# Kernel tuning notes

Hardware: AMD Instinct MI355X
Metric: run time of the kernel (lower is better)

## Reference

```python
import jax, jax.numpy as jnp
import numpy as np

T, B, H = 512, 64, 512
GRAD_CLIP = 1.0


def setup_inputs() -> dict:
    key = jax.random.key(0)
    k_x, k_r, k_wi, k_wh = jax.random.split(key, 4)
    xs = jax.random.normal(k_x, (T, B, H), dtype=jnp.float32)
    resets = jax.random.randint(k_r, (T, B), 0, 2).astype(bool)
    c0 = jnp.zeros((B, H), dtype=jnp.float32)
    h0 = jnp.zeros((B, H), dtype=jnp.float32)
    scale = 1.0 / np.sqrt(H)
    # fused gate weights, gate order [i, f, g, o] (flax LSTMCell convention)
    Wi = jax.random.normal(k_wi, (H, 4 * H), dtype=jnp.float32) * scale
    Wh = jax.random.normal(k_wh, (H, 4 * H), dtype=jnp.float32) * scale
    # flax LSTMCell: input dense has no bias, hidden dense has bias with
    # forget-gate bias initialized to ones
    b = jnp.zeros((4 * H,), dtype=jnp.float32).at[H:2 * H].set(1.0)
    return {"xs": xs, "resets": resets, "c0": c0, "h0": h0,
            "Wi": Wi, "Wh": Wh, "b": b}


def _clip_st(t):
    # straight-through clip: forward value is clipped, gradient is identity
    return t + jax.lax.stop_gradient(jnp.clip(t, -GRAD_CLIP, GRAD_CLIP) - t)


def reference(xs, resets, c0, h0, Wi, Wh, b):
    def step(carry, inp):
        c, h = carry
        x, r = inp  # x: [B,H], r: [B] bool
        m = r[:, None]
        c = jnp.where(m, jnp.zeros_like(c), c)
        h = jnp.where(m, jnp.zeros_like(h), h)
        z = x @ Wi + h @ Wh + b  # [B, 4H]
        i, f, g, o = jnp.split(z, 4, axis=-1)
        i = jax.nn.sigmoid(i)
        f = jax.nn.sigmoid(f)
        g = jnp.tanh(g)
        o = jax.nn.sigmoid(o)
        nc = f * c + i * g
        nh = o * jnp.tanh(nc)
        nc = _clip_st(nc)
        nh = _clip_st(nh)  # y == clipped new_h; clipping is idempotent on values
        return (nc, nh), nh

    (cf, hf), ys = jax.lax.scan(step, (c0, h0), (xs, resets))
    return ys  # [T, B, H]
```

## Files before the change

### kernel.cpp

```cpp
#include <hip/hip_runtime.h>

#define T_ 512
#define B_ 64
#define H_ 512
#define LMAX 20
#define NROWS (T_*B_)

typedef _Float16 f16;
typedef __attribute__((ext_vector_type(2))) _Float16 f16x2;
typedef __attribute__((ext_vector_type(8))) _Float16 f16x8;
typedef __attribute__((ext_vector_type(4))) float fx4;

#define M_CNT 0
#define M_OFF 32

__device__ __forceinline__ float sigm(float z)  { return 1.0f / (1.0f + __expf(-z)); }
__device__ __forceinline__ float tanha(float z) { return 2.0f / (1.0f + __expf(-2.0f * z)) - 1.0f; }

__global__ __launch_bounds__(256) void k_prepw(const float* __restrict__ Wi,
                                               const float* __restrict__ Wh,
                                               f16* __restrict__ W2t) {
    __shared__ float tile[64][65];
    const int c0  = blockIdx.x * 64;
    const int k20 = blockIdx.y * 64;
    const int tid = threadIdx.x;
    #pragma unroll
    for (int s = 0; s < 16; s++) {
        int k2r = s * 4 + (tid >> 6);
        int c   = tid & 63;
        int k2  = k20 + k2r;
        float v = (k2 < H_) ? Wi[(size_t)k2 * 2048 + c0 + c]
                            : Wh[(size_t)(k2 - H_) * 2048 + c0 + c];
        tile[c][k2r] = v;
    }
    __syncthreads();
    const int c  = tid >> 2;
    const int ch = tid & 3;
    f16 tmp[16];
    #pragma unroll
    for (int u = 0; u < 16; u++) tmp[u] = (f16)tile[c][ch * 16 + u];
    f16* dst = W2t + (size_t)(c0 + c) * 1024 + k20 + ch * 16;
    *(uint4*)(dst)     = *(const uint4*)(tmp);
    *(uint4*)(dst + 8) = *(const uint4*)(tmp + 8);
}

__global__ __launch_bounds__(256) void k_scan_build(const int* __restrict__ resets,
                                                    int* __restrict__ lvl,
                                                    int* __restrict__ meta,
                                                    int* __restrict__ rowid,
                                                    int* __restrict__ rmap) {
    __shared__ unsigned long long mask[T_];
    __shared__ int cnt[LMAX + 1][B_];
    __shared__ int cur[LMAX + 1][B_];
    __shared__ int cntk[LMAX + 1], offk[LMAX + 1];

    const int tid  = threadIdx.x;
    const int lane = tid & 63;
    const int wave = tid >> 6;

    for (int t = wave; t < T_; t += 4) {
        int r = resets[t * B_ + lane];
        unsigned long long m = __ballot(r != 0);
        if (lane == 0) mask[t] = m;
    }
    for (int i = tid; i < (LMAX + 1) * B_; i += 256) ((int*)cnt)[i] = 0;
    __syncthreads();

    if (tid < B_) {
        const int b = tid;
        int prev = 0;
        for (int t = 0; t < T_; t++) {
            int rst = (int)((mask[t] >> b) & 1ULL);
            int lv = (t == 0) ? 0 : (rst ? 0 : prev + 1);
            int kk = lv < LMAX ? lv : LMAX;
            cnt[kk][b] += 1;
            lvl[t * B_ + b] = lv;
            prev = lv;
        }
    }
    __syncthreads();

    if (tid <= LMAX) {
        const int k = tid;
        int acc = 0;
        for (int b = 0; b < B_; b++) { cur[k][b] = acc; acc += cnt[k][b]; }
        cntk[k] = acc;
    }
    __syncthreads();
    if (tid == 0) {
        int acc = 0;
        for (int k = 0; k <= LMAX; k++) { offk[k] = acc; acc += cntk[k]; }
    }
    __syncthreads();
    if (tid <= LMAX) {
        const int k = tid;
        for (int b = 0; b < B_; b++) cur[k][b] += offk[k];
        meta[M_CNT + k] = cntk[k];
        meta[M_OFF + k] = offk[k];
    }
    __syncthreads();

    if (tid < B_) {
        const int b = tid;
        int prev = 0;
        for (int t = 0; t < T_; t++) {
            int rst = (int)((mask[t] >> b) & 1ULL);
            int lv = (t == 0) ? 0 : (rst ? 0 : prev + 1);
            int kk = lv < LMAX ? lv : LMAX;
            int r = cur[kk][b];
            cur[kk][b] = r + 1;
            int tb = t * B_ + b;
            rowid[tb] = r;
            rmap[r] = tb;
            prev = lv;
        }
    }
}


__global__ __launch_bounds__(256) void k_xcast(const float* __restrict__ xs,
                                               f16* __restrict__ X) {
    int gid = blockIdx.x * 256 + threadIdx.x;
    const float4* src = (const float4*)(xs) + (size_t)gid * 2;
    float4 a = src[0], c = src[1];
    f16x8 o;
    o[0]=(f16)a.x; o[1]=(f16)a.y; o[2]=(f16)a.z; o[3]=(f16)a.w;
    o[4]=(f16)c.x; o[5]=(f16)c.y; o[6]=(f16)c.z; o[7]=(f16)c.w;
    *(f16x8*)(X + (size_t)gid * 8) = o;
}

__global__ __launch_bounds__(256) void k_hz0(const float* __restrict__ h0,
                                             const f16* __restrict__ W2t,
                                             float* __restrict__ hz0) {
    const int b = blockIdx.x >> 3;
    const int j = ((blockIdx.x & 7) * 256) + threadIdx.x;
    __shared__ float h[H_];
    for (int k = threadIdx.x; k < H_; k += 256) h[k] = h0[b * H_ + k];
    __syncthreads();
    const f16* wr = W2t + (size_t)j * 1024 + 512;
    float acc = 0.f;
    for (int k = 0; k < H_; k += 8) {
        f16x8 w = *(const f16x8*)(wr + k);
        #pragma unroll
        for (int u = 0; u < 8; u++) acc += h[k + u] * (float)w[u];
    }
    hz0[(size_t)b * 2048 + j] = acc;
}

__global__ __launch_bounds__(256) void k_xz(const f16* __restrict__ X,
                                            const f16* __restrict__ W2t,
                                            f16* __restrict__ XZ) {
    const int r0 = blockIdx.x * 128;
    const int j0 = blockIdx.y * 128;
    __shared__ __align__(16) f16 As[128][40];
    __shared__ __align__(16) f16 Bs[128][40];
    const int tid  = threadIdx.x;
    const int lane = tid & 63;
    const int wave = tid >> 6;
    const int wm = wave & 1, wn = wave >> 1;
    const int n = lane & 15, q = lane >> 4;

    fx4 acc[4][4];
    #pragma unroll
    for (int i = 0; i < 4; i++)
        #pragma unroll
        for (int jj = 0; jj < 4; jj++) acc[i][jj] = (fx4){0.f,0.f,0.f,0.f};

    const int arow = tid >> 2, ach = tid & 3;
    const f16* xa = X + (size_t)(r0 + arow) * 512 + ach * 8;
    const f16* xb = X + (size_t)(r0 + 64 + arow) * 512 + ach * 8;
    const f16* wa = W2t + (size_t)(j0 + arow) * 1024 + ach * 8;
    const f16* wb = W2t + (size_t)(j0 + 64 + arow) * 1024 + ach * 8;

    for (int k0 = 0; k0 < 512; k0 += 32) {
        *(uint4*)(&As[arow][ach * 8])      = *(const uint4*)(xa + k0);
        *(uint4*)(&As[64 + arow][ach * 8]) = *(const uint4*)(xb + k0);
        *(uint4*)(&Bs[arow][ach * 8])      = *(const uint4*)(wa + k0);
        *(uint4*)(&Bs[64 + arow][ach * 8]) = *(const uint4*)(wb + k0);
        __syncthreads();
        f16x8 af[4], bf[4];
        #pragma unroll
        for (int mt = 0; mt < 4; mt++) af[mt] = *(const f16x8*)(&As[wm*64 + mt*16 + n][q*8]);
        #pragma unroll
        for (int nt = 0; nt < 4; nt++) bf[nt] = *(const f16x8*)(&Bs[wn*64 + nt*16 + n][q*8]);
        #pragma unroll
        for (int mt = 0; mt < 4; mt++)
            #pragma unroll
            for (int nt = 0; nt < 4; nt++)
                acc[mt][nt] = __builtin_amdgcn_mfma_f32_16x16x32_f16(af[mt], bf[nt], acc[mt][nt], 0, 0, 0);
        __syncthreads();
    }
    #pragma unroll
    for (int mt = 0; mt < 4; mt++)
        #pragma unroll
        for (int nt = 0; nt < 4; nt++)
            #pragma unroll
            for (int reg = 0; reg < 4; reg++) {
                int row = r0 + wm * 64 + mt * 16 + q * 4 + reg;
                int col = j0 + wn * 64 + nt * 16 + n;
                XZ[(size_t)row * 2048 + col] = (f16)acc[mt][nt][reg];
            }
}

__global__ __launch_bounds__(256) void k_lvl0epi(
    const f16* __restrict__ XZ, const float* __restrict__ hz0,
    const float* __restrict__ c0, const float* __restrict__ bias,
    const int* __restrict__ resets, const int* __restrict__ meta,
    const int* __restrict__ rmap, const int* __restrict__ rowid,
    f16* __restrict__ Hb, f16* __restrict__ Cb, float* __restrict__ ys)
{
    const int r = blockIdx.x;
    if (r >= meta[M_CNT + 0]) return;
    const int tb = rmap[r];
    const int t = tb >> 6, b = tb & 63;
    const bool useinit = (t == 0) && (resets[b] == 0);
    int s = -1;
    if (t + 1 < T_ && resets[tb + B_] == 0) s = rowid[tb + B_];

    const int jh = threadIdx.x * 2;
    const f16* zr = XZ + (size_t)tb * 2048;
    f16x2 vi = *(const f16x2*)(zr + jh);
    f16x2 vf = *(const f16x2*)(zr + H_ + jh);
    f16x2 vg = *(const f16x2*)(zr + 2 * H_ + jh);
    f16x2 vo = *(const f16x2*)(zr + 3 * H_ + jh);

    float nhv[2], ncv[2];
    #pragma unroll
    for (int u = 0; u < 2; u++) {
        int j = jh + u;
        float zi = (float)vi[u] + bias[j];
        float zf = (float)vf[u] + bias[H_ + j];
        float zg = (float)vg[u] + bias[2 * H_ + j];
        float zo = (float)vo[u] + bias[3 * H_ + j];
        float cp = 0.f;
        if (useinit) {
            const float* hzr = hz0 + (size_t)b * 2048;
            zi += hzr[j]; zf += hzr[H_ + j]; zg += hzr[2 * H_ + j]; zo += hzr[3 * H_ + j];
            cp = c0[b * H_ + j];
        }
        float iv = sigm(zi), fv = sigm(zf), gv = tanha(zg), ov = sigm(zo);
        float nc = fv * cp + iv * gv;
        float nh = ov * tanha(nc);
        ncv[u] = fminf(1.f, fmaxf(-1.f, nc));
        nhv[u] = fminf(1.f, fmaxf(-1.f, nh));
        ys[(size_t)tb * H_ + j] = nhv[u];
    }
    if (s >= 0) {
        f16x2 hv, cv;
        hv[0] = (f16)nhv[0]; hv[1] = (f16)nhv[1];
        cv[0] = (f16)ncv[0]; cv[1] = (f16)ncv[1];
        *(f16x2*)(Hb + (size_t)s * H_ + jh) = hv;
        *(f16x2*)(Cb + (size_t)s * H_ + jh) = cv;
    }
}

__global__ __launch_bounds__(256) void k_levelh(
    int level,
    const int* __restrict__ resets,
    const f16* __restrict__ W2t,
    const float* __restrict__ bias,
    const f16* __restrict__ XZ,
    f16* __restrict__ Hb,
    f16* __restrict__ Cb,
    const int* __restrict__ meta,
    const int* __restrict__ rmap,
    const int* __restrict__ rowid,
    float* __restrict__ ys)
{
    const int cnt = meta[M_CNT + level];
    const int row0 = blockIdx.x * 64;
    if (row0 >= cnt) return;
    const int off = meta[M_OFF + level];
    const int j0 = blockIdx.y * 64;

    __shared__ __align__(16) f16 As[64][40];
    __shared__ __align__(16) f16 Ws[256][40];

    const int tid  = threadIdx.x;
    const int lane = tid & 63;
    const int wave = tid >> 6;
    const int n = lane & 15;
    const int q = lane >> 4;

    fx4 acc[16];
    #pragma unroll
    for (int i = 0; i < 16; i++) acc[i] = (fx4){0.f, 0.f, 0.f, 0.f};

    const int ar  = tid >> 2;
    const int ach = tid & 3;
    const int gr_stage = row0 + ar;
    const int srow = off + (gr_stage < cnt ? gr_stage : 0);
    const f16* agp = Hb + (size_t)srow * H_ + ach * 8;
    const int wc = tid >> 2;

    for (int k0 = 0; k0 < 512; k0 += 32) {
        *(uint4*)(&As[ar][ach * 8]) = *(const uint4*)(agp + k0);
        #pragma unroll
        for (int s = 0; s < 4; s++) {
            const f16* wp = W2t + (size_t)(s * H_ + j0 + wc) * 1024 + 512 + k0 + ach * 8;
            *(uint4*)(&Ws[s * 64 + wc][ach * 8]) = *(const uint4*)wp;
        }
        __syncthreads();
        f16x8 a = *(const f16x8*)(&As[wave * 16 + n][q * 8]);
        #pragma unroll
        for (int ct = 0; ct < 16; ct++) {
            f16x8 bb = *(const f16x8*)(&Ws[ct * 16 + n][q * 8]);
            acc[ct] = __builtin_amdgcn_mfma_f32_16x16x32_f16(a, bb, acc[ct], 0, 0, 0);
        }
        __syncthreads();
    }

    int tbs[4], succs[4], grows[4], valids[4];
    #pragma unroll
    for (int reg = 0; reg < 4; reg++) {
        int gr = row0 + wave * 16 + q * 4 + reg;
        valids[reg] = (gr < cnt);
        int grow = off + (gr < cnt ? gr : 0);
        grows[reg] = grow;
        int tb = rmap[grow];
        tbs[reg] = tb;
        int s = -1;
        if (gr < cnt && (tb >> 6) + 1 < T_ && resets[tb + B_] == 0) s = rowid[tb + B_];
        succs[reg] = s;
    }
    #pragma unroll
    for (int jt = 0; jt < 4; jt++) {
        int j = j0 + jt * 16 + n;
        float b_i = bias[j], b_f = bias[H_ + j], b_g = bias[2 * H_ + j], b_o = bias[3 * H_ + j];
        #pragma unroll
        for (int reg = 0; reg < 4; reg++) {
            if (!valids[reg]) continue;
            const f16* zr = XZ + (size_t)tbs[reg] * 2048;
            float zi = acc[jt][reg]      + b_i + (float)zr[j];
            float zf = acc[4 + jt][reg]  + b_f + (float)zr[H_ + j];
            float zg = acc[8 + jt][reg]  + b_g + (float)zr[2 * H_ + j];
            float zo = acc[12 + jt][reg] + b_o + (float)zr[3 * H_ + j];
            float cp = (float)Cb[(size_t)grows[reg] * H_ + j];
            float iv = sigm(zi), fv = sigm(zf), gv = tanha(zg), ov = sigm(zo);
            float nc = fv * cp + iv * gv;
            float nh = ov * tanha(nc);
            float ncc = fminf(1.f, fmaxf(-1.f, nc));
            float nhc = fminf(1.f, fmaxf(-1.f, nh));
            ys[(size_t)tbs[reg] * H_ + j] = nhc;
            int s = succs[reg];
            if (s >= 0) {
                Hb[(size_t)s * H_ + j] = (f16)nhc;
                Cb[(size_t)s * H_ + j] = (f16)ncc;
            }
        }
    }
}


__global__ __launch_bounds__(256) void k_fill(const float* __restrict__ xs,
                                              const float* __restrict__ c0,
                                              const float* __restrict__ h0,
                                              const int* __restrict__ resets,
                                              const int* __restrict__ rmap,
                                              const int* __restrict__ meta,
                                              f16* __restrict__ A,
                                              f16* __restrict__ Cb) {
    int gid = blockIdx.x * 256 + threadIdx.x;
    int r = gid >> 6, seg = gid & 63;
    int tb = rmap[r];
    const float4* src = (const float4*)(xs + (size_t)tb * H_ + seg * 8);
    float4 a = src[0];
    float4 c = src[1];
    f16x8 o;
    o[0]=(f16)a.x; o[1]=(f16)a.y; o[2]=(f16)a.z; o[3]=(f16)a.w;
    o[4]=(f16)c.x; o[5]=(f16)c.y; o[6]=(f16)c.z; o[7]=(f16)c.w;
    *(f16x8*)(A + (size_t)r * 1024 + seg * 8) = o;

    if (r < meta[M_CNT + 0]) {
        int t = tb >> 6, b = tb & 63;
        bool useinit = (t == 0) && (resets[b] == 0);
        f16x8 hv, cv;
        #pragma unroll
        for (int u = 0; u < 8; u++) {
            int j = seg * 8 + u;
            hv[u] = (f16)(useinit ? h0[b * H_ + j] : 0.0f);
            cv[u] = (f16)(useinit ? c0[b * H_ + j] : 0.0f);
        }
        *(f16x8*)(A + (size_t)r * 1024 + H_ + seg * 8) = hv;
        *(f16x8*)(Cb + (size_t)r * H_ + seg * 8) = cv;
    }
}

__global__ __launch_bounds__(256) void k_level(
    int level,
    const int* __restrict__ resets,
    const f16* __restrict__ W2t,
    const float* __restrict__ bias,
    f16* __restrict__ Ab,
    f16* __restrict__ Cb,
    const int* __restrict__ meta,
    const int* __restrict__ rmap,
    const int* __restrict__ rowid,
    float* __restrict__ ys)
{
    const int cnt = meta[M_CNT + level];
    const int row0 = blockIdx.x * 64;
    if (row0 >= cnt) return;
    const int off = meta[M_OFF + level];
    const int j0 = blockIdx.y * 64;

    __shared__ __align__(16) f16 As[64][40];
    __shared__ __align__(16) f16 Ws[256][40];

    const int tid  = threadIdx.x;
    const int lane = tid & 63;
    const int wave = tid >> 6;
    const int n = lane & 15;
    const int q = lane >> 4;

    fx4 acc[16];
    #pragma unroll
    for (int i = 0; i < 16; i++) acc[i] = (fx4){0.f, 0.f, 0.f, 0.f};

    const int ar  = tid >> 2;
    const int ach = tid & 3;
    const int gr_stage = row0 + ar;
    const int srow = off + (gr_stage < cnt ? gr_stage : 0);
    const f16* agp = Ab + (size_t)srow * 1024 + ach * 8;
    const int wc = tid >> 2;

    for (int k0 = 0; k0 < 1024; k0 += 32) {
        *(uint4*)(&As[ar][ach * 8]) = *(const uint4*)(agp + k0);
        #pragma unroll
        for (int s = 0; s < 4; s++) {
            const f16* wp = W2t + (size_t)(s * H_ + j0 + wc) * 1024 + k0 + ach * 8;
            *(uint4*)(&Ws[s * 64 + wc][ach * 8]) = *(const uint4*)wp;
        }
        __syncthreads();
        f16x8 a = *(const f16x8*)(&As[wave * 16 + n][q * 8]);
        #pragma unroll
        for (int ct = 0; ct < 16; ct++) {
            f16x8 bb = *(const f16x8*)(&Ws[ct * 16 + n][q * 8]);
            acc[ct] = __builtin_amdgcn_mfma_f32_16x16x32_f16(a, bb, acc[ct], 0, 0, 0);
        }
        __syncthreads();
    }

    int tbs[4], succs[4], grows[4], valids[4];
    #pragma unroll
    for (int reg = 0; reg < 4; reg++) {
        int gr = row0 + wave * 16 + q * 4 + reg;
        valids[reg] = (gr < cnt);
        int grow = off + (gr < cnt ? gr : 0);
        grows[reg] = grow;
        int tb = rmap[grow];
        tbs[reg] = tb;
        int s = -1;
        if (gr < cnt && (tb >> 6) + 1 < T_ && resets[tb + B_] == 0) s = rowid[tb + B_];
        succs[reg] = s;
    }
    #pragma unroll
    for (int jt = 0; jt < 4; jt++) {
        int j = j0 + jt * 16 + n;
        float b_i = bias[j], b_f = bias[H_ + j], b_g = bias[2 * H_ + j], b_o = bias[3 * H_ + j];
        #pragma unroll
        for (int reg = 0; reg < 4; reg++) {
            if (!valids[reg]) continue;
            float zi = acc[jt][reg] + b_i;
            float zf = acc[4 + jt][reg] + b_f;
            float zg = acc[8 + jt][reg] + b_g;
            float zo = acc[12 + jt][reg] + b_o;
            float cp = (float)Cb[(size_t)grows[reg] * H_ + j];
            float iv = sigm(zi), fv = sigm(zf), gv = tanha(zg), ov = sigm(zo);
            float nc = fv * cp + iv * gv;
            float nh = ov * tanha(nc);
            float ncc = fminf(1.f, fmaxf(-1.f, nc));
            float nhc = fminf(1.f, fmaxf(-1.f, nh));
            ys[(size_t)tbs[reg] * H_ + j] = nhc;
            int s = succs[reg];
            if (s >= 0) {
                Ab[(size_t)s * 1024 + H_ + j] = (f16)nhc;
                Cb[(size_t)s * H_ + j] = (f16)ncc;
            }
        }
    }
}

__global__ __launch_bounds__(256) void k_cleanup(
    const float* __restrict__ xs, const float* __restrict__ Wi,
    const float* __restrict__ Wh, const float* __restrict__ bias,
    const int* __restrict__ rowid, const int* __restrict__ meta,
    const int* __restrict__ rmap,
    const f16* __restrict__ Cb, float* __restrict__ ys)
{
    const int cntL = meta[M_CNT + LMAX];
    if (cntL == 0) return;
    const int offL = meta[M_OFF + LMAX];
    const int b = blockIdx.x;
    const int tid = threadIdx.x;
    __shared__ float hs[H_], cs[H_];
    int last_t = -2;
    for (int idx = 0; idx < cntL; idx++) {
        const int tb = rmap[offL + idx];
        if ((tb & 63) != b) continue;
        const int t = tb >> 6;
        if (t != last_t + 1) {
            for (int j = tid; j < H_; j += 256) {
                hs[j] = ys[(size_t)(tb - B_) * H_ + j];
                cs[j] = (float)Cb[(size_t)rowid[tb] * H_ + j];
            }
        }
        __syncthreads();
        float nh_[2], nc_[2];
        #pragma unroll
        for (int u = 0; u < 2; u++) {
            int j = tid + u * 256;
            float zi = bias[j], zf = bias[H_ + j], zg = bias[2 * H_ + j], zo = bias[3 * H_ + j];
            const float* xr = xs + (size_t)tb * H_;
            for (int k = 0; k < H_; k++) {
                float xk = xr[k], hk = hs[k];
                zi += xk * Wi[(size_t)k * 2048 + j]          + hk * Wh[(size_t)k * 2048 + j];
                zf += xk * Wi[(size_t)k * 2048 + H_ + j]     + hk * Wh[(size_t)k * 2048 + H_ + j];
                zg += xk * Wi[(size_t)k * 2048 + 2 * H_ + j] + hk * Wh[(size_t)k * 2048 + 2 * H_ + j];
                zo += xk * Wi[(size_t)k * 2048 + 3 * H_ + j] + hk * Wh[(size_t)k * 2048 + 3 * H_ + j];
            }
            float cp = cs[j];
            float iv = sigm(zi), fv = sigm(zf), gv = tanha(zg), ov = sigm(zo);
            float nc = fv * cp + iv * gv;
            float nh = ov * tanha(nc);
            nc_[u] = fminf(1.f, fmaxf(-1.f, nc));
            nh_[u] = fminf(1.f, fmaxf(-1.f, nh));
            ys[(size_t)tb * H_ + j] = nh_[u];
        }
        __syncthreads();
        #pragma unroll
        for (int u = 0; u < 2; u++) { int j = tid + u * 256; hs[j] = nh_[u]; cs[j] = nc_[u]; }
        last_t = t;
    }
}

__global__ __launch_bounds__(256) void k_fb_init(const float* __restrict__ c0,
                                                 const float* __restrict__ h0,
                                                 float* __restrict__ cbuf,
                                                 float* __restrict__ hA) {
    int idx = blockIdx.x * 256 + threadIdx.x;
    if (idx >= B_ * H_) return;
    cbuf[idx] = c0[idx];
    hA[idx] = h0[idx];
}

__global__ __launch_bounds__(256) void k_fb_step(
    int t,
    const float* __restrict__ xs, const int* __restrict__ resets,
    const float* __restrict__ Wi, const float* __restrict__ Wh,
    const float* __restrict__ bias,
    const float* __restrict__ hin, float* __restrict__ hout,
    float* __restrict__ cbuf, float* __restrict__ ys)
{
    int idx = blockIdx.x * 256 + threadIdx.x;
    int b = idx >> 9, j = idx & 511;
    int tb = t * B_ + b;
    bool rst = resets[tb] != 0;
    float zi = bias[j], zf = bias[H_ + j], zg = bias[2 * H_ + j], zo = bias[3 * H_ + j];
    const float* xr = xs + (size_t)tb * H_;
    for (int k = 0; k < H_; k++) {
        float xk = xr[k];
        zi += xk * Wi[(size_t)k * 2048 + j];
        zf += xk * Wi[(size_t)k * 2048 + H_ + j];
        zg += xk * Wi[(size_t)k * 2048 + 2 * H_ + j];
        zo += xk * Wi[(size_t)k * 2048 + 3 * H_ + j];
    }
    if (!rst) {
        const float* hr = hin + b * H_;
        for (int k = 0; k < H_; k++) {
            float hk = hr[k];
            zi += hk * Wh[(size_t)k * 2048 + j];
            zf += hk * Wh[(size_t)k * 2048 + H_ + j];
            zg += hk * Wh[(size_t)k * 2048 + 2 * H_ + j];
            zo += hk * Wh[(size_t)k * 2048 + 3 * H_ + j];
        }
    }
    float cp = rst ? 0.f : cbuf[idx];
    float iv = sigm(zi), fv = sigm(zf), gv = tanha(zg), ov = sigm(zo);
    float nc = fv * cp + iv * gv;
    float nh = ov * tanha(nc);
    float ncc = fminf(1.f, fmaxf(-1.f, nc));
    float nhc = fminf(1.f, fmaxf(-1.f, nh));
    cbuf[idx] = ncc;
    hout[idx] = nhc;
    ys[(size_t)tb * H_ + j] = nhc;
}

extern "C" void kernel_launch(void* const* d_in, const int* in_sizes, int n_in,
                              void* d_out, int out_size, void* d_ws, size_t ws_size,
                              hipStream_t stream) {
    const float* xs    = (const float*)d_in[0];
    const int*   resets= (const int*)d_in[1];
    const float* c0    = (const float*)d_in[2];
    const float* h0    = (const float*)d_in[3];
    const float* Wi    = (const float*)d_in[4];
    const float* Wh    = (const float*)d_in[5];
    const float* bias  = (const float*)d_in[6];
    float* ys = (float*)d_out;
    char* ws = (char*)d_ws;

    const size_t A_W2T  = 0;
    const size_t A_X    = A_W2T + (size_t)4*1024*1024;
    const size_t A_XZ   = A_X   + (size_t)32*1024*1024;
    const size_t A_HB   = A_XZ  + (size_t)128*1024*1024;
    const size_t A_CB   = A_HB  + (size_t)32*1024*1024;
    const size_t A_HZ0  = A_CB  + (size_t)32*1024*1024;
    const size_t A_LVL  = A_HZ0 + (size_t)512*1024;
    const size_t A_RID  = A_LVL + 131072;
    const size_t A_RMAP = A_RID + 131072;
    const size_t A_META = A_RMAP + 131072;
    const size_t NEEDED_A = A_META + 512;

    const size_t B_A    = 0;
    const size_t B_C    = 67108864;
    const size_t B_W2T  = 100663296;
    const size_t B_LVL  = 104857600;
    const size_t B_RID  = 104988672;
    const size_t B_RMAP = 105119744;
    const size_t B_META = 105250816;
    const size_t NEEDED_B = 105251328;

    if (ws_size >= NEEDED_A) {
        f16* W2t  = (f16*)(ws + A_W2T);
        f16* X    = (f16*)(ws + A_X);
        f16* XZ   = (f16*)(ws + A_XZ);
        f16* Hb   = (f16*)(ws + A_HB);
        f16* Cb   = (f16*)(ws + A_CB);
        float* hz0= (float*)(ws + A_HZ0);
        int* lvl  = (int*)(ws + A_LVL);
        int* rid  = (int*)(ws + A_RID);
        int* rmap = (int*)(ws + A_RMAP);
        int* meta = (int*)(ws + A_META);

        k_prepw<<<dim3(32, 16), dim3(256), 0, stream>>>(Wi, Wh, W2t);
        k_scan_build<<<dim3(1), dim3(256), 0, stream>>>(resets, lvl, meta, rid, rmap);
        k_xcast<<<dim3(NROWS * 64 / 256 / 8 * 8), dim3(256), 0, stream>>>(xs, X);
        k_hz0<<<dim3(512), dim3(256), 0, stream>>>(h0, W2t, hz0);
        k_xz<<<dim3(NROWS / 128, 16), dim3(256), 0, stream>>>(X, W2t, XZ);
        k_lvl0epi<<<dim3(NROWS), dim3(256), 0, stream>>>(XZ, hz0, c0, bias, resets,
                                                         meta, rmap, rid, Hb, Cb, ys);
        for (int k = 1; k < LMAX; k++) {
            int maxr = 64 * ((512 + k) / (k + 1));
            dim3 grid((maxr + 63) / 64, 8);
            k_levelh<<<grid, dim3(256), 0, stream>>>(k, resets, W2t, bias, XZ, Hb, Cb,
                                                     meta, rmap, rid, ys);
        }
        k_cleanup<<<dim3(64), dim3(256), 0, stream>>>(xs, Wi, Wh, bias, rid, meta, rmap, Cb, ys);
    } else if (ws_size >= NEEDED_B) {
        f16* A    = (f16*)(ws + B_A);
        f16* Cb   = (f16*)(ws + B_C);
        f16* W2t  = (f16*)(ws + B_W2T);
        int* lvl  = (int*)(ws + B_LVL);
        int* rid  = (int*)(ws + B_RID);
        int* rmap = (int*)(ws + B_RMAP);
        int* meta = (int*)(ws + B_META);

        k_prepw<<<dim3(32, 16), dim3(256), 0, stream>>>(Wi, Wh, W2t);
        k_scan_build<<<dim3(1), dim3(256), 0, stream>>>(resets, lvl, meta, rid, rmap);
        k_fill<<<dim3(NROWS * 64 / 256), dim3(256), 0, stream>>>(xs, c0, h0, resets, rmap, meta, A, Cb);
        for (int k = 0; k < LMAX; k++) {
            int maxr = 64 * ((512 + k) / (k + 1));
            dim3 grid((maxr + 63) / 64, 8);
            k_level<<<grid, dim3(256), 0, stream>>>(k, resets, W2t, bias, A, Cb,
                                                    meta, rmap, rid, ys);
        }
        k_cleanup<<<dim3(64), dim3(256), 0, stream>>>(xs, Wi, Wh, bias, rid, meta, rmap, Cb, ys);
    } else {
        float* cbuf = (float*)(ws);
        float* hA   = (float*)(ws + 131072);
        float* hB   = (float*)(ws + 262144);
        k_fb_init<<<dim3(128), dim3(256), 0, stream>>>(c0, h0, cbuf, hA);
        for (int t = 0; t < T_; t++) {
            const float* hin = (t & 1) ? hB : hA;
            float* hout      = (t & 1) ? hA : hB;
            k_fb_step<<<dim3(128), dim3(256), 0, stream>>>(t, xs, resets, Wi, Wh, bias,
                                                           hin, hout, cbuf, ys);
        }
    }
}
```

Before: 850.4 us.

## Fuse level-0 epilogue and per-level recurrence kernels into one cooperative persistent kernel

Replaces the level-0 epilogue launch and the series of per-level recurrence launches with a single cooperative kernel. It processes each reset-depth level in grid-stride tiles and separates levels with grid-wide syncs. It also records the deepest non-empty level, so levels that do not occur are skipped rather than launched empty. The aim is to remove roughly twenty kernel launches and their idle gaps. In exchange it adds grid barrier costs, a smaller persistent grid per level, and host occupancy and device-property queries on every call.

```diff
diff --git a/kernel.cpp b/kernel.cpp
--- a/kernel.cpp
+++ b/kernel.cpp
@@ -1,4 +1,7 @@
 #include <hip/hip_runtime.h>
+#include <hip/hip_cooperative_groups.h>
+
+namespace cg = cooperative_groups;
 
 #define T_ 512
 #define B_ 64
@@ -13,6 +16,7 @@
 
 #define M_CNT 0
 #define M_OFF 32
+#define M_MAXL 64
 
 __device__ __forceinline__ float sigm(float z)  { return 1.0f / (1.0f + __expf(-z)); }
 __device__ __forceinline__ float tanha(float z) { return 2.0f / (1.0f + __expf(-2.0f * z)) - 1.0f; }
@@ -88,8 +92,12 @@
     }
     __syncthreads();
     if (tid == 0) {
-        int acc = 0;
-        for (int k = 0; k <= LMAX; k++) { offk[k] = acc; acc += cntk[k]; }
+        int acc = 0, ml = 0;
+        for (int k = 0; k <= LMAX; k++) {
+            offk[k] = acc; acc += cntk[k];
+            if (cntk[k] > 0) ml = k;
+        }
+        meta[M_MAXL] = ml;
     }
     __syncthreads();
     if (tid <= LMAX) {
@@ -200,6 +208,163 @@
                 int col = j0 + wn * 64 + nt * 16 + n;
                 XZ[(size_t)row * 2048 + col] = (f16)acc[mt][nt][reg];
             }
+}
+
+__global__ __launch_bounds__(256) void k_levels(
+    const int* __restrict__ resets,
+    const f16* __restrict__ W2t,
+    const float* __restrict__ bias,
+    const f16* __restrict__ XZ,
+    const float* __restrict__ hz0,
+    const float* __restrict__ c0,
+    f16* __restrict__ Hb,
+    f16* __restrict__ Cb,
+    const int* __restrict__ meta,
+    const int* __restrict__ rmap,
+    const int* __restrict__ rowid,
+    float* __restrict__ ys)
+{
+    cg::grid_group gg = cg::this_grid();
+    __shared__ __align__(16) f16 As[64][40];
+    __shared__ __align__(16) f16 Ws[256][40];
+
+    const int tid  = threadIdx.x;
+    const int lane = tid & 63;
+    const int wave = tid >> 6;
+    const int n = lane & 15;
+    const int q = lane >> 4;
+
+    {
+        const int cnt0 = meta[M_CNT + 0];
+        for (int r = blockIdx.x; r < cnt0; r += gridDim.x) {
+            const int tb = rmap[r];
+            const int t = tb >> 6, b = tb & 63;
+            const bool useinit = (t == 0) && (resets[b] == 0);
+            int s = -1;
+            if (t + 1 < T_ && resets[tb + B_] == 0) s = rowid[tb + B_];
+            const int jh = tid * 2;
+            const f16* zr = XZ + (size_t)tb * 2048;
+            f16x2 vi = *(const f16x2*)(zr + jh);
+            f16x2 vf = *(const f16x2*)(zr + H_ + jh);
+            f16x2 vg = *(const f16x2*)(zr + 2 * H_ + jh);
+            f16x2 vo = *(const f16x2*)(zr + 3 * H_ + jh);
+            float nhv[2], ncv[2];
+            #pragma unroll
+            for (int u = 0; u < 2; u++) {
+                int j = jh + u;
+                float zi = (float)vi[u] + bias[j];
+                float zf = (float)vf[u] + bias[H_ + j];
+                float zg = (float)vg[u] + bias[2 * H_ + j];
+                float zo = (float)vo[u] + bias[3 * H_ + j];
+                float cp = 0.f;
+                if (useinit) {
+                    const float* hzr = hz0 + (size_t)b * 2048;
+                    zi += hzr[j]; zf += hzr[H_ + j]; zg += hzr[2 * H_ + j]; zo += hzr[3 * H_ + j];
+                    cp = c0[b * H_ + j];
+                }
+                float iv = sigm(zi), fv = sigm(zf), gv = tanha(zg), ov = sigm(zo);
+                float nc = fv * cp + iv * gv;
+                float nh = ov * tanha(nc);
+                ncv[u] = fminf(1.f, fmaxf(-1.f, nc));
+                nhv[u] = fminf(1.f, fmaxf(-1.f, nh));
+                ys[(size_t)tb * H_ + j] = nhv[u];
+            }
+            if (s >= 0) {
+                f16x2 hv, cv;
+                hv[0] = (f16)nhv[0]; hv[1] = (f16)nhv[1];
+                cv[0] = (f16)ncv[0]; cv[1] = (f16)ncv[1];
+                *(f16x2*)(Hb + (size_t)s * H_ + jh) = hv;
+                *(f16x2*)(Cb + (size_t)s * H_ + jh) = cv;
+            }
+        }
+    }
+    __threadfence();
+    gg.sync();
+    __threadfence();
+
+    const int maxl = meta[M_MAXL];
+    const int kend = maxl < (LMAX - 1) ? maxl : (LMAX - 1);
+
+    for (int k = 1; k <= kend; k++) {
+        const int cnt = meta[M_CNT + k];
+        const int off = meta[M_OFF + k];
+        const int tiles = ((cnt + 63) >> 6) * 8;
+        for (int tile = blockIdx.x; tile < tiles; tile += gridDim.x) {
+            const int row0 = (tile >> 3) * 64;
+            const int j0   = (tile & 7) * 64;
+
+            fx4 acc[16];
+            #pragma unroll
+            for (int i = 0; i < 16; i++) acc[i] = (fx4){0.f, 0.f, 0.f, 0.f};
+
+            const int ar  = tid >> 2;
+            const int ach = tid & 3;
+            const int gr_stage = row0 + ar;
+            const int srow = off + (gr_stage < cnt ? gr_stage : 0);
+            const f16* agp = Hb + (size_t)srow * H_ + ach * 8;
+            const int wc = tid >> 2;
+
+            for (int k0 = 0; k0 < 512; k0 += 32) {
+                *(uint4*)(&As[ar][ach * 8]) = *(const uint4*)(agp + k0);
+                #pragma unroll
+                for (int s = 0; s < 4; s++) {
+                    const f16* wp = W2t + (size_t)(s * H_ + j0 + wc) * 1024 + 512 + k0 + ach * 8;
+                    *(uint4*)(&Ws[s * 64 + wc][ach * 8]) = *(const uint4*)wp;
+                }
+                __syncthreads();
+                f16x8 a = *(const f16x8*)(&As[wave * 16 + n][q * 8]);
+                #pragma unroll
+                for (int ct = 0; ct < 16; ct++) {
+                    f16x8 bb = *(const f16x8*)(&Ws[ct * 16 + n][q * 8]);
+                    acc[ct] = __builtin_amdgcn_mfma_f32_16x16x32_f16(a, bb, acc[ct], 0, 0, 0);
+                }
+                __syncthreads();
+            }
+
+            int tbs[4], succs[4], grows[4], valids[4];
+            #pragma unroll
+            for (int reg = 0; reg < 4; reg++) {
+                int gr = row0 + wave * 16 + q * 4 + reg;
+                valids[reg] = (gr < cnt);
+                int grow = off + (gr < cnt ? gr : 0);
+                grows[reg] = grow;
+                int tb = rmap[grow];
+                tbs[reg] = tb;
+                int s = -1;
+                if (gr < cnt && (tb >> 6) + 1 < T_ && resets[tb + B_] == 0) s = rowid[tb + B_];
+                succs[reg] = s;
+            }
+            #pragma unroll
+            for (int jt = 0; jt < 4; jt++) {
+                int j = j0 + jt * 16 + n;
+                float b_i = bias[j], b_f = bias[H_ + j], b_g = bias[2 * H_ + j], b_o = bias[3 * H_ + j];
+                #pragma unroll
+                for (int reg = 0; reg < 4; reg++) {
+                    if (!valids[reg]) continue;
+                    const f16* zr = XZ + (size_t)tbs[reg] * 2048;
+                    float zi = acc[jt][reg]      + b_i + (float)zr[j];
+                    float zf = acc[4 + jt][reg]  + b_f + (float)zr[H_ + j];
+                    float zg = acc[8 + jt][reg]  + b_g + (float)zr[2 * H_ + j];
+                    float zo = acc[12 + jt][reg] + b_o + (float)zr[3 * H_ + j];
+                    float cp = (float)Cb[(size_t)grows[reg] * H_ + j];
+                    float iv = sigm(zi), fv = sigm(zf), gv = tanha(zg), ov = sigm(zo);
+                    float nc = fv * cp + iv * gv;
+                    float nh = ov * tanha(nc);
+                    float ncc = fminf(1.f, fmaxf(-1.f, nc));
+                    float nhc = fminf(1.f, fmaxf(-1.f, nh));
+                    ys[(size_t)tbs[reg] * H_ + j] = nhc;
+                    int s = succs[reg];
+                    if (s >= 0) {
+                        Hb[(size_t)s * H_ + j] = (f16)nhc;
+                        Cb[(size_t)s * H_ + j] = (f16)ncc;
+                    }
+                }
+            }
+        }
+        __threadfence();
+        gg.sync();
+        __threadfence();
+    }
 }
 
 __global__ __launch_bounds__(256) void k_lvl0epi(
@@ -637,13 +802,39 @@
         k_xcast<<<dim3(NROWS * 64 / 256 / 8 * 8), dim3(256), 0, stream>>>(xs, X);
         k_hz0<<<dim3(512), dim3(256), 0, stream>>>(h0, W2t, hz0);
         k_xz<<<dim3(NROWS / 128, 16), dim3(256), 0, stream>>>(X, W2t, XZ);
-        k_lvl0epi<<<dim3(NROWS), dim3(256), 0, stream>>>(XZ, hz0, c0, bias, resets,
-                                                         meta, rmap, rid, Hb, Cb, ys);
-        for (int k = 1; k < LMAX; k++) {
-            int maxr = 64 * ((512 + k) / (k + 1));
-            dim3 grid((maxr + 63) / 64, 8);
-            k_levelh<<<grid, dim3(256), 0, stream>>>(k, resets, W2t, bias, XZ, Hb, Cb,
-                                                     meta, rmap, rid, ys);
+
+        bool coop_ok = false;
+        int occ = 0;
+        if (hipOccupancyMaxActiveBlocksPerMultiprocessor(&occ, (const void*)k_levels, 256, 0)
+                == hipSuccess && occ >= 1) {
+            int ncu = 256;
+            hipDeviceProp_t prop;
+            int dev = 0;
+            if (hipGetDevice(&dev) == hipSuccess &&
+                hipGetDeviceProperties(&prop, dev) == hipSuccess)
+                ncu = prop.multiProcessorCount;
+            long long g = (long long)occ * ncu;
+            if (g > 2048) g = 2048;
+            const int* resets_a = resets; const f16* W2t_a = W2t; const float* bias_a = bias;
+            const f16* XZ_a = XZ; const float* hz0_a = hz0; const float* c0_a = c0;
+            f16* Hb_a = Hb; f16* Cb_a = Cb; const int* meta_a = meta;
+            const int* rmap_a = rmap; const int* rid_a = rid; float* ys_a = ys;
+            void* args[] = { (void*)&resets_a, (void*)&W2t_a, (void*)&bias_a,
+                             (void*)&XZ_a, (void*)&hz0_a, (void*)&c0_a,
+                             (void*)&Hb_a, (void*)&Cb_a, (void*)&meta_a,
+                             (void*)&rmap_a, (void*)&rid_a, (void*)&ys_a };
+            coop_ok = (hipLaunchCooperativeKernel((const void*)k_levels, dim3((unsigned)g),
+                                                  dim3(256), args, 0, stream) == hipSuccess);
+        }
+        if (!coop_ok) {
+            k_lvl0epi<<<dim3(NROWS), dim3(256), 0, stream>>>(XZ, hz0, c0, bias, resets,
+                                                             meta, rmap, rid, Hb, Cb, ys);
+            for (int k = 1; k < LMAX; k++) {
+                int maxr = 64 * ((512 + k) / (k + 1));
+                dim3 grid((maxr + 63) / 64, 8);
+                k_levelh<<<grid, dim3(256), 0, stream>>>(k, resets, W2t, bias, XZ, Hb, Cb,
+                                                         meta, rmap, rid, ys);
+            }
         }
         k_cleanup<<<dim3(64), dim3(256), 0, stream>>>(xs, Wi, Wh, bias, rid, meta, rmap, Cb, ys);
     } else if (ws_size >= NEEDED_B) {
```

Result: slower. 2.136 ms (+151.1%).
